# Kernel optimization log

Measured on AMD Instinct MI355X. Metric: run time of the kernel, lower is better.

The kernel has to match this reference:

```python
import jax, jax.numpy as jnp
import numpy as np

LN_EPS = 1e-5


def setup_inputs() -> dict:
    key = jax.random.key(0)
    k1, k2, k3, k4 = jax.random.split(key, 4)
    N, D, E = 10000, 512, 150000
    scale = 1.0 / np.sqrt(D)
    return {
        "node_feature": jax.random.normal(k1, (N, D), dtype=jnp.float32),
        "edge_index": jax.random.randint(k2, (2, E), 0, N, dtype=jnp.int64),
        "ln_gamma": jnp.ones((D,), dtype=jnp.float32),
        "ln_beta": jnp.zeros((D,), dtype=jnp.float32),
        "w_l": jax.random.normal(k3, (D, D), dtype=jnp.float32) * scale,
        "b_l": jnp.zeros((D,), dtype=jnp.float32),
        "w_r": jax.random.normal(k4, (D, D), dtype=jnp.float32) * scale,
    }


def reference(node_feature, edge_index, ln_gamma, ln_beta, w_l, b_l, w_r):
    N = node_feature.shape[0]
    residual = node_feature

    # LayerNorm over feature dim
    mu = jnp.mean(node_feature, axis=-1, keepdims=True)
    var = jnp.mean(jnp.square(node_feature - mu), axis=-1, keepdims=True)
    x = (node_feature - mu) * jax.lax.rsqrt(var + LN_EPS) * ln_gamma + ln_beta

    # SAGEConv (mean aggr): gather x_j from src, segment-mean into dst
    src, dst = edge_index[0], edge_index[1]
    msg = x[src]                                   # [E, D]
    summed = jax.ops.segment_sum(msg, dst, num_segments=N)        # [N, D]
    cnt = jax.ops.segment_sum(jnp.ones_like(dst, dtype=x.dtype), dst, num_segments=N)
    agg = summed / jnp.maximum(cnt, 1.0)[:, None]

    # out = lin_l(agg) + lin_r(x)  (lin_r has no bias in PyG SAGEConv)
    out = agg @ w_l.T + b_l + x @ w_r.T
    out = jax.nn.relu(out)
    # dropout is identity in eval mode
    return out + residual
```

## Files before the change

### kernel.cpp

```cpp
#include <hip/hip_runtime.h>
#include <hip/hip_bf16.h>

typedef float f32x4 __attribute__((ext_vector_type(4)));
typedef __bf16 bf16x8 __attribute__((ext_vector_type(8)));
typedef unsigned short u16x8 __attribute__((ext_vector_type(8)));

#define N_NODES 10000
#define DIM 512
#define MPAD 10112
#define DEGCAP 96

__global__ __launch_bounds__(256) void zero_kernel(int* __restrict__ cnt) {
    cnt[blockIdx.x * 256 + threadIdx.x] = 0;
}

__global__ __launch_bounds__(256) void phase1_kernel(
    const float* __restrict__ wl, const float* __restrict__ wr,
    __hip_bfloat16* __restrict__ W,
    const float* __restrict__ xin, const float* __restrict__ gamma,
    const float* __restrict__ beta, __hip_bfloat16* __restrict__ A,
    const int* __restrict__ eidx, int* __restrict__ cnt, int* __restrict__ adj,
    int E, int fill_start) {
    int b = blockIdx.x;
    int tid = threadIdx.x;

    if (b < 512) {
        int idx = b * 256 + tid;
        int base = idx * 4;
        int d = base >> 10;
        int k = base & 1023;
        const float* src = (k < 512) ? (wl + d * 512 + k) : (wr + d * 512 + (k - 512));
        float4 v = *(const float4*)src;
        __hip_bfloat16* o = W + (size_t)d * 1024 + k;
        o[0] = __float2bfloat16(v.x);
        o[1] = __float2bfloat16(v.y);
        o[2] = __float2bfloat16(v.z);
        o[3] = __float2bfloat16(v.w);
    } else if (b < fill_start) {
        int row = (b - 512) * 4 + (tid >> 6);
        int lane = tid & 63;
        const float* xr = xin + (size_t)row * DIM + lane * 8;
        float4 v0 = *(const float4*)xr;
        float4 v1 = *(const float4*)(xr + 4);
        float s  = v0.x + v0.y + v0.z + v0.w + v1.x + v1.y + v1.z + v1.w;
        float ss = v0.x*v0.x + v0.y*v0.y + v0.z*v0.z + v0.w*v0.w
                 + v1.x*v1.x + v1.y*v1.y + v1.z*v1.z + v1.w*v1.w;
        #pragma unroll
        for (int o = 32; o > 0; o >>= 1) {
            s  += __shfl_xor(s, o, 64);
            ss += __shfl_xor(ss, o, 64);
        }
        float mu  = s * (1.0f / 512.0f);
        float var = ss * (1.0f / 512.0f) - mu * mu;
        float rstd = rsqrtf(var + 1e-5f);
        float4 g0 = *(const float4*)(gamma + lane * 8);
        float4 g1 = *(const float4*)(gamma + lane * 8 + 4);
        float4 b0 = *(const float4*)(beta + lane * 8);
        float4 b1 = *(const float4*)(beta + lane * 8 + 4);
        __hip_bfloat16* a = A + (size_t)row * 1024 + 512 + lane * 8;
        a[0] = __float2bfloat16((v0.x - mu) * rstd * g0.x + b0.x);
        a[1] = __float2bfloat16((v0.y - mu) * rstd * g0.y + b0.y);
        a[2] = __float2bfloat16((v0.z - mu) * rstd * g0.z + b0.z);
        a[3] = __float2bfloat16((v0.w - mu) * rstd * g0.w + b0.w);
        a[4] = __float2bfloat16((v1.x - mu) * rstd * g1.x + b1.x);
        a[5] = __float2bfloat16((v1.y - mu) * rstd * g1.y + b1.y);
        a[6] = __float2bfloat16((v1.z - mu) * rstd * g1.z + b1.z);
        a[7] = __float2bfloat16((v1.w - mu) * rstd * g1.w + b1.w);
    } else {
        int i = (b - fill_start) * 256 + tid;
        if (i < E) {
            int dst = eidx[E + i];
            int src = eidx[i];
            int pos = atomicAdd(&cnt[dst], 1);
            if (pos < DEGCAP) adj[dst * DEGCAP + pos] = src;
        }
    }
}

__global__ __launch_bounds__(256) void gather_kernel(const int* __restrict__ cnt,
                                                     const int* __restrict__ adj,
                                                     __hip_bfloat16* __restrict__ A) {
    int gw = (blockIdx.x * 256 + threadIdx.x) >> 6;
    int lane = threadIdx.x & 63;
    int deg = cnt[gw];
    const int* al = adj + gw * DEGCAP;
    float acc0[8] = {}, acc1[8] = {};
    int j = 0;
    for (; j + 4 <= deg; j += 4) {
        int a0 = al[j], a1 = al[j + 1], a2 = al[j + 2], a3 = al[j + 3];
        u16x8 v0 = *(const u16x8*)(A + (size_t)a0 * 1024 + 512 + lane * 8);
        u16x8 v1 = *(const u16x8*)(A + (size_t)a1 * 1024 + 512 + lane * 8);
        u16x8 v2 = *(const u16x8*)(A + (size_t)a2 * 1024 + 512 + lane * 8);
        u16x8 v3 = *(const u16x8*)(A + (size_t)a3 * 1024 + 512 + lane * 8);
        #pragma unroll
        for (int k = 0; k < 8; ++k) {
            acc0[k] += __uint_as_float((unsigned)v0[k] << 16)
                     + __uint_as_float((unsigned)v1[k] << 16);
            acc1[k] += __uint_as_float((unsigned)v2[k] << 16)
                     + __uint_as_float((unsigned)v3[k] << 16);
        }
    }
    for (; j < deg; ++j) {
        int a0 = al[j];
        u16x8 v0 = *(const u16x8*)(A + (size_t)a0 * 1024 + 512 + lane * 8);
        #pragma unroll
        for (int k = 0; k < 8; ++k)
            acc0[k] += __uint_as_float((unsigned)v0[k] << 16);
    }
    float sc = 1.0f / fmaxf((float)deg, 1.0f);
    __hip_bfloat16* o = A + (size_t)gw * 1024 + lane * 8;
    #pragma unroll
    for (int k = 0; k < 8; ++k)
        o[k] = __float2bfloat16((acc0[k] + acc1[k]) * sc);
}

__global__ __launch_bounds__(256) void gemm_kernel(const __hip_bfloat16* __restrict__ A,
                                                   const __hip_bfloat16* __restrict__ Wb,
                                                   const float* __restrict__ bias,
                                                   const float* __restrict__ resid,
                                                   float* __restrict__ out) {
    __shared__ __hip_bfloat16 As[2][64 * 32];
    __shared__ __hip_bfloat16 Bs[2][128 * 32];
    const int tid = threadIdx.x;
    const int lane = tid & 63;
    const int w = tid >> 6;
    const int wr = w >> 1, wc = w & 1;

    int bid = blockIdx.x;
    int tl = (bid & 7) * 79 + (bid >> 3);
    int mx = tl >> 2, ny = tl & 3;
    const size_t arow0 = (size_t)mx * 64;
    const size_t bcol0 = (size_t)ny * 128;

    f32x4 acc[2][4] = {};

    const int rsw = ((lane & 15) >> 1) & 3;
    const int csw = (((lane >> 4) ^ rsw) & 3) * 8;

#define STAGE(buf, t)                                                                \
    {                                                                                \
        int r = tid >> 2, sl = tid & 3;                                              \
        int c8 = sl ^ ((r >> 1) & 3);                                                \
        const __hip_bfloat16* ga = A + (size_t)(arow0 + r) * 1024 + (t) * 32 + c8 * 8; \
        __builtin_amdgcn_global_load_lds(                                            \
            (const __attribute__((address_space(1))) void*)ga,                       \
            (__attribute__((address_space(3))) void*)(As[buf] + tid * 8), 16, 0, 0); \
        _Pragma("unroll")                                                            \
        for (int it = 0; it < 2; ++it) {                                             \
            int j = tid + it * 256;                                                  \
            int rb = j >> 2, slb = j & 3;                                            \
            int cb8 = slb ^ ((rb >> 1) & 3);                                         \
            const __hip_bfloat16* gb = Wb + (size_t)(bcol0 + rb) * 1024 + (t) * 32 + cb8 * 8; \
            __builtin_amdgcn_global_load_lds(                                        \
                (const __attribute__((address_space(1))) void*)gb,                   \
                (__attribute__((address_space(3))) void*)(Bs[buf] + j * 8), 16, 0, 0); \
        }                                                                            \
    }

    STAGE(0, 0)
    __syncthreads();

    for (int t = 0; t < 32; ++t) {
        int p = t & 1;
        if (t + 1 < 32) STAGE(p ^ 1, t + 1)

        bf16x8 af[2], bfr[4];
        #pragma unroll
        for (int m = 0; m < 2; ++m)
            af[m] = *(const bf16x8*)(As[p] + (wr * 32 + m * 16 + (lane & 15)) * 32 + csw);
        #pragma unroll
        for (int n = 0; n < 4; ++n)
            bfr[n] = *(const bf16x8*)(Bs[p] + (wc * 64 + n * 16 + (lane & 15)) * 32 + csw);
        #pragma unroll
        for (int m = 0; m < 2; ++m)
            #pragma unroll
            for (int n = 0; n < 4; ++n)
                acc[m][n] = __builtin_amdgcn_mfma_f32_16x16x32_bf16(af[m], bfr[n], acc[m][n], 0, 0, 0);
        __syncthreads();
    }
#undef STAGE

    #pragma unroll
    for (int m = 0; m < 2; ++m) {
        int rowb = (int)arow0 + wr * 32 + m * 16 + (lane >> 4) * 4;
        #pragma unroll
        for (int n = 0; n < 4; ++n) {
            int col = (int)bcol0 + wc * 64 + n * 16 + (lane & 15);
            float bv = bias[col];
            #pragma unroll
            for (int j = 0; j < 4; ++j) {
                int row = rowb + j;
                if (row < N_NODES) {
                    float v = acc[m][n][j] + bv;
                    v = v > 0.0f ? v : 0.0f;
                    out[(size_t)row * 512 + col] = v + resid[(size_t)row * 512 + col];
                }
            }
        }
    }
}

extern "C" void kernel_launch(void* const* d_in, const int* in_sizes, int n_in,
                              void* d_out, int out_size, void* d_ws, size_t ws_size,
                              hipStream_t stream) {
    const float* node  = (const float*)d_in[0];
    const int*   eidx  = (const int*)d_in[1];
    const float* gamma = (const float*)d_in[2];
    const float* beta  = (const float*)d_in[3];
    const float* wl    = (const float*)d_in[4];
    const float* bl    = (const float*)d_in[5];
    const float* wr    = (const float*)d_in[6];
    float* out = (float*)d_out;
    const int E = in_sizes[1] / 2;

    char* ws = (char*)d_ws;
    int* cnt = (int*)ws;
    int* adj = cnt + 10240;
    size_t adj_bytes = ((size_t)N_NODES * DEGCAP * 4 + 255) & ~(size_t)255;
    __hip_bfloat16* A = (__hip_bfloat16*)((char*)adj + adj_bytes);
    __hip_bfloat16* W = (__hip_bfloat16*)((char*)A + (size_t)MPAD * 1024 * 2);

    const int fill_start = 512 + 2500;
    const int nFill = (E + 255) / 256;

    zero_kernel<<<40, 256, 0, stream>>>(cnt);
    phase1_kernel<<<fill_start + nFill, 256, 0, stream>>>(
        wl, wr, W, node, gamma, beta, A, eidx, cnt, adj, E, fill_start);
    gather_kernel<<<(N_NODES * 64) / 256, 256, 0, stream>>>(cnt, adj, A);
    gemm_kernel<<<632, 256, 0, stream>>>(A, W, bl, node, out);
}
```

Before: 78.61 us.

## Split gather across four column-quarter blocks with XCD-aware node mapping

```diff
diff --git a/kernel.cpp b/kernel.cpp
--- a/kernel.cpp
+++ b/kernel.cpp
@@ -80,38 +80,41 @@
 __global__ __launch_bounds__(256) void gather_kernel(const int* __restrict__ cnt,
                                                      const int* __restrict__ adj,
                                                      __hip_bfloat16* __restrict__ A) {
-    int gw = (blockIdx.x * 256 + threadIdx.x) >> 6;
+    int b = blockIdx.x;
+    int x = b & 7;
+    int t = b >> 3;
+    int q = x & 3;
+    int half = x >> 2;
+    int node = ((half * 1250 + t) << 2) + (threadIdx.x >> 6);
     int lane = threadIdx.x & 63;
-    int deg = cnt[gw];
-    const int* al = adj + gw * DEGCAP;
-    float acc0[8] = {}, acc1[8] = {};
+    int deg = cnt[node];
+    const int* al = adj + node * DEGCAP;
+    const char* Abase = (const char*)A;
+    size_t coff = 1024 + (size_t)q * 256 + lane * 4;
+    float a0 = 0.f, a1 = 0.f;
     int j = 0;
     for (; j + 4 <= deg; j += 4) {
-        int a0 = al[j], a1 = al[j + 1], a2 = al[j + 2], a3 = al[j + 3];
-        u16x8 v0 = *(const u16x8*)(A + (size_t)a0 * 1024 + 512 + lane * 8);
-        u16x8 v1 = *(const u16x8*)(A + (size_t)a1 * 1024 + 512 + lane * 8);
-        u16x8 v2 = *(const u16x8*)(A + (size_t)a2 * 1024 + 512 + lane * 8);
-        u16x8 v3 = *(const u16x8*)(A + (size_t)a3 * 1024 + 512 + lane * 8);
-        #pragma unroll
-        for (int k = 0; k < 8; ++k) {
-            acc0[k] += __uint_as_float((unsigned)v0[k] << 16)
-                     + __uint_as_float((unsigned)v1[k] << 16);
-            acc1[k] += __uint_as_float((unsigned)v2[k] << 16)
-                     + __uint_as_float((unsigned)v3[k] << 16);
-        }
+        int n0 = al[j], n1 = al[j + 1], n2 = al[j + 2], n3 = al[j + 3];
+        unsigned v0 = *(const unsigned*)(Abase + (size_t)n0 * 2048 + coff);
+        unsigned v1 = *(const unsigned*)(Abase + (size_t)n1 * 2048 + coff);
+        unsigned v2 = *(const unsigned*)(Abase + (size_t)n2 * 2048 + coff);
+        unsigned v3 = *(const unsigned*)(Abase + (size_t)n3 * 2048 + coff);
+        a0 += __uint_as_float(v0 << 16) + __uint_as_float(v1 << 16)
+            + __uint_as_float(v2 << 16) + __uint_as_float(v3 << 16);
+        a1 += __uint_as_float(v0 & 0xffff0000u) + __uint_as_float(v1 & 0xffff0000u)
+            + __uint_as_float(v2 & 0xffff0000u) + __uint_as_float(v3 & 0xffff0000u);
     }
     for (; j < deg; ++j) {
-        int a0 = al[j];
-        u16x8 v0 = *(const u16x8*)(A + (size_t)a0 * 1024 + 512 + lane * 8);
-        #pragma unroll
-        for (int k = 0; k < 8; ++k)
-            acc0[k] += __uint_as_float((unsigned)v0[k] << 16);
+        unsigned v0 = *(const unsigned*)(Abase + (size_t)al[j] * 2048 + coff);
+        a0 += __uint_as_float(v0 << 16);
+        a1 += __uint_as_float(v0 & 0xffff0000u);
     }
     float sc = 1.0f / fmaxf((float)deg, 1.0f);
-    __hip_bfloat16* o = A + (size_t)gw * 1024 + lane * 8;
-    #pragma unroll
-    for (int k = 0; k < 8; ++k)
-        o[k] = __float2bfloat16((acc0[k] + acc1[k]) * sc);
+    __hip_bfloat16 r0 = __float2bfloat16(a0 * sc);
+    __hip_bfloat16 r1 = __float2bfloat16(a1 * sc);
+    __hip_bfloat16* o = (__hip_bfloat16*)((char*)A + (size_t)node * 2048 + (size_t)q * 256 + lane * 4);
+    o[0] = r0;
+    o[1] = r1;
 }
 
 __global__ __launch_bounds__(256) void gemm_kernel(const __hip_bfloat16* __restrict__ A,
@@ -226,6 +229,6 @@
     zero_kernel<<<40, 256, 0, stream>>>(cnt);
     phase1_kernel<<<fill_start + nFill, 256, 0, stream>>>(
         wl, wr, W, node, gamma, beta, A, eidx, cnt, adj, E, fill_start);
-    gather_kernel<<<(N_NODES * 64) / 256, 256, 0, stream>>>(cnt, adj, A);
+    gather_kernel<<<10000, 256, 0, stream>>>(cnt, adj, A);
     gemm_kernel<<<632, 256, 0, stream>>>(A, W, bl, node, out);
 }
```

Result: no change. 79.76 us (+1.5%).
